# Kernel optimization log

Hardware: AMD Instinct MI355X
Metric: run time of the kernel (lower is better)

The kernel has to match this reference:

```python
import jax, jax.numpy as jnp
import numpy as np

EPS = 1e-5  # BatchNorm2d default eps

def setup_inputs() -> dict:
    key = jax.random.key(0)
    k1, k2, k3, k4 = jax.random.split(key, 4)
    B, Cin, Cout, T, V = 64, 64, 128, 300, 25
    x = jax.random.normal(k1, (B, Cin, T, V), dtype=jnp.float32)
    adj = jax.random.uniform(k2, (V, V), dtype=jnp.float32)
    # Conv2d(kernel_size=1) weight (Cout, Cin), kaiming-ish scale
    W = jax.random.normal(k3, (Cout, Cin), dtype=jnp.float32) * (1.0 / np.sqrt(Cin))
    b = jnp.zeros((Cout,), dtype=jnp.float32)
    gamma = jnp.ones((Cout,), dtype=jnp.float32)
    beta = jnp.zeros((Cout,), dtype=jnp.float32)
    return {"x": x, "adj": adj, "W": W, "b": b, "gamma": gamma, "beta": beta}

def reference(x, adj, W, b, gamma, beta):
    # x: (B, C, T, V); graph aggregation over joints: matmul with adj on last dim
    xg = jnp.einsum('bctv,vw->bctw', x, adj)
    # 1x1 conv == per-(t,v) channel projection
    y = jnp.einsum('bctv,oc->botv', xg, W) + b[None, :, None, None]
    # BatchNorm2d (training mode): per-channel stats over (B, T, V), biased var
    mean = jnp.mean(y, axis=(0, 2, 3), keepdims=True)
    var = jnp.mean((y - mean) ** 2, axis=(0, 2, 3), keepdims=True)
    yn = (y - mean) * jax.lax.rsqrt(var + EPS)
    out = jax.nn.relu(gamma[None, :, None, None] * yn + beta[None, :, None, None])
    return out
```

## Files before the change

### kernel.cpp

```cpp
#include <hip/hip_runtime.h>
#include <stdint.h>

typedef __attribute__((ext_vector_type(8)))  short   short8;
typedef __attribute__((ext_vector_type(4)))  short   short4v;
typedef __attribute__((ext_vector_type(16))) float   floatx16;

#define B_    64
#define CIN   64
#define COUT  128
#define T_    300
#define V_    25
#define TV    (T_ * V_)
#define NRED  (B_ * T_ * V_)
#define NSLOTS 32
#define EPS   1e-5f


__device__ __forceinline__ unsigned short f2bf(float f) {
    union { float f; uint32_t u; } c; c.f = f;
    uint32_t u = c.u;
    u += 0x7FFFu + ((u >> 16) & 1u);
    return (unsigned short)(u >> 16);
}

__device__ __forceinline__ floatx16 fzero16() {
    floatx16 z;
#pragma unroll
    for (int i = 0; i < 16; ++i) z[i] = 0.f;
    return z;
}

__global__ void pack_kernel(const float* __restrict__ W, const float* __restrict__ adj,
                            unsigned short* __restrict__ wsW, unsigned short* __restrict__ wsAdj) {
    int stride = blockDim.x * gridDim.x;
    for (int idx = threadIdx.x + blockIdx.x * blockDim.x; idx < 8192; idx += stride) {
        int j  = idx & 7;
        int l  = (idx >> 3) & 63;
        int kk = (idx >> 9) & 3;
        int w  = idx >> 11;
        int o  = 32 * w + (l & 31);
        int c  = 16 * kk + 8 * (l >> 5) + j;
        wsW[idx] = f2bf(W[o * CIN + c]);
    }
    for (int idx = threadIdx.x + blockIdx.x * blockDim.x; idx < 1024; idx += stride) {
        int j = idx & 7;
        int l = (idx >> 3) & 63;
        int s = idx >> 9;
        int k = 16 * s + 8 * (l >> 5) + j;
        int n = l & 31;
        float v = (k < V_ && n < V_) ? adj[k * V_ + n] : 0.f;
        wsAdj[idx] = f2bf(v);
    }
}

template <bool WRITE>
__global__ __launch_bounds__(256) void main_kernel(
    const float* __restrict__ x,
    const unsigned short* __restrict__ wsW,
    const unsigned short* __restrict__ wsAdj,
    const float* __restrict__ scale, const float* __restrict__ shift,
    float* __restrict__ psum, float* __restrict__ psq,
    float* __restrict__ out)
{
    __shared__ unsigned short Gbuf[2][2048] __attribute__((aligned(16)));

    const int tid  = threadIdx.x;
    const int wave = tid >> 6;
    const int lane = tid & 63;
    const int q    = lane >> 5;
    const int ln   = lane & 31;
    const int b    = blockIdx.y;
    const int t0   = blockIdx.x * 4;
    const int ctile = wave & 1;
    const int tsel  = wave >> 1;

    short8 wf[4];
#pragma unroll
    for (int kk = 0; kk < 4; ++kk)
        wf[kk] = ((const short8*)wsW)[(wave * 4 + kk) * 64 + lane];
    short8 af[2];
#pragma unroll
    for (int s = 0; s < 2; ++s)
        af[s] = ((const short8*)wsAdj)[s * 64 + lane];

    float sc[16], sh[16], sums[16], sqs[16];
    if (WRITE) {
#pragma unroll
        for (int r = 0; r < 16; ++r) {
            int row = 32 * wave + (r & 3) + 8 * (r >> 2) + 4 * q;
            sc[r] = scale[row];
            sh[r] = shift[row];
        }
    } else {
#pragma unroll
        for (int r = 0; r < 16; ++r) { sums[r] = 0.f; sqs[r] = 0.f; }
    }

    for (int iter = 0; iter < 2; ++iter) {
        const int t = t0 + iter * 2 + tsel;
        const float* xrow = x + ((size_t)(b * CIN + 32 * ctile + ln) * T_ + t) * V_;

        short8 xa0, xa1;
#pragma unroll
        for (int j = 0; j < 8; ++j) xa0[j] = (short)f2bf(xrow[8 * q + j]);
        if (q == 0) {
#pragma unroll
            for (int j = 0; j < 8; ++j) xa1[j] = (short)f2bf(xrow[16 + j]);
        } else {
            xa1[0] = (short)f2bf(xrow[24]);
#pragma unroll
            for (int j = 1; j < 8; ++j) xa1[j] = 0;
        }

        floatx16 g = fzero16();
        g = __builtin_amdgcn_mfma_f32_32x32x16_bf16(xa0, af[0], g, 0, 0, 0);
        g = __builtin_amdgcn_mfma_f32_32x32x16_bf16(xa1, af[1], g, 0, 0, 0);

        __syncthreads();

#pragma unroll
        for (int r1 = 0; r1 < 4; ++r1) {
            short4v p;
#pragma unroll
            for (int r0 = 0; r0 < 4; ++r0) p[r0] = (short)f2bf(g[r1 * 4 + r0]);
            *(short4v*)&Gbuf[tsel][((4 * ctile + r1) * 32 + ln) * 8 + 4 * q] = p;
        }

        __syncthreads();

#pragma unroll
        for (int ts = 0; ts < 2; ++ts) {
            floatx16 acc = fzero16();
#pragma unroll
            for (int kk = 0; kk < 4; ++kk) {
                short8 bfrag = *(const short8*)&Gbuf[ts][((kk * 2 + q) * 32 + ln) * 8];
                acc = __builtin_amdgcn_mfma_f32_32x32x16_bf16(wf[kk], bfrag, acc, 0, 0, 0);
            }
            if (WRITE) {
                const int t_out = t0 + iter * 2 + ts;
                if (ln < V_) {
                    float* obase = out + ((size_t)(b * COUT + 32 * wave) * T_ + t_out) * V_ + ln;
#pragma unroll
                    for (int r = 0; r < 16; ++r) {
                        int row = (r & 3) + 8 * (r >> 2) + 4 * q;
                        float v = sc[r] * acc[r] + sh[r];
                        obase[(size_t)row * TV] = v > 0.f ? v : 0.f;
                    }
                }
            } else {
#pragma unroll
                for (int r = 0; r < 16; ++r) {
                    sums[r] += acc[r];
                    sqs[r]  += acc[r] * acc[r];
                }
            }
        }
    }

    if (!WRITE) {
#pragma unroll
        for (int r = 0; r < 16; ++r) {
            float s = sums[r], ss = sqs[r];
#pragma unroll
            for (int m = 1; m <= 16; m <<= 1) {
                s  += __shfl_xor(s,  m, 64);
                ss += __shfl_xor(ss, m, 64);
            }
            sums[r] = s; sqs[r] = ss;
        }
        if (ln == 0) {
            int slot = (blockIdx.y * 75 + blockIdx.x) & (NSLOTS - 1);
#pragma unroll
            for (int r = 0; r < 16; ++r) {
                int ch = 32 * wave + (r & 3) + 8 * (r >> 2) + 4 * q;
                atomicAdd(&psum[slot * COUT + ch], sums[r]);
                atomicAdd(&psq [slot * COUT + ch], sqs[r]);
            }
        }
    }
}

__global__ void stats_kernel(const float* __restrict__ psum, const float* __restrict__ psq,
                             const float* __restrict__ gamma, const float* __restrict__ beta,
                             float* __restrict__ scale, float* __restrict__ shift) {
    int o = threadIdx.x;
    float s = 0.f, ss = 0.f;
    for (int k = 0; k < NSLOTS; ++k) {
        s  += psum[k * COUT + o];
        ss += psq [k * COUT + o];
    }
    float mean = s / (float)NRED;
    float var  = ss / (float)NRED - mean * mean;
    float inv  = rsqrtf(var + EPS);
    float scv  = gamma[o] * inv;
    scale[o] = scv;
    shift[o] = beta[o] - mean * scv;
}

extern "C" void kernel_launch(void* const* d_in, const int* in_sizes, int n_in,
                              void* d_out, int out_size, void* d_ws, size_t ws_size,
                              hipStream_t stream) {
    const float* x     = (const float*)d_in[0];
    const float* adj   = (const float*)d_in[1];
    const float* W     = (const float*)d_in[2];
    const float* gamma = (const float*)d_in[4];
    const float* beta  = (const float*)d_in[5];
    float* out = (float*)d_out;

    char* ws = (char*)d_ws;
    unsigned short* wsW   = (unsigned short*)(ws);
    unsigned short* wsAdj = (unsigned short*)(ws + 16384);
    float* psum  = (float*)(ws + 18432);
    float* psq   = (float*)(ws + 34816);
    float* scale = (float*)(ws + 51200);
    float* shift = (float*)(ws + 51712);

    hipMemsetAsync(psum, 0, 2 * NSLOTS * COUT * sizeof(float), stream);

    pack_kernel<<<8, 256, 0, stream>>>(W, adj, wsW, wsAdj);

    dim3 grid(75, 64);
    main_kernel<false><<<grid, 256, 0, stream>>>(x, wsW, wsAdj, nullptr, nullptr, psum, psq, nullptr);
    stats_kernel<<<1, 128, 0, stream>>>(psum, psq, gamma, beta, scale, shift);
    main_kernel<true><<<grid, 256, 0, stream>>>(x, wsW, wsAdj, scale, shift, psum, psq, out);
}
```

Before: 464.6 us.

## Reorder to channel projection before graph aggregation, fuse packing and stats kernels

Computes W·x first and then multiplies by adj (associativity), keeping the intermediate in registers and rearranging it across lanes with a shuffle, which removes the LDS buffer and its barriers. Weight and adjacency fragments are built inside each kernel, so the pack kernel goes away, and the stats reduction is folded into the second pass, removing the stats kernel. Each block now covers 12 timesteps instead of 4, and output stores are vectorized along the joint dimension. The trade-offs are extra shuffles and redundant stats and fragment work per block, plus strided scalar loads of x.

```diff
diff --git a/kernel.cpp b/kernel.cpp
--- a/kernel.cpp
+++ b/kernel.cpp
@@ -1,26 +1,26 @@
 #include <hip/hip_runtime.h>
+#include <hip/hip_bf16.h>
 #include <stdint.h>
 
 typedef __attribute__((ext_vector_type(8)))  short   short8;
-typedef __attribute__((ext_vector_type(4)))  short   short4v;
 typedef __attribute__((ext_vector_type(16))) float   floatx16;
+typedef __attribute__((ext_vector_type(4)))  float   floatx4;
 
 #define B_    64
 #define CIN   64
 #define COUT  128
 #define T_    300
 #define V_    25
-#define TV    (T_ * V_)
 #define NRED  (B_ * T_ * V_)
 #define NSLOTS 32
+#define NT    12
 #define EPS   1e-5f
 
 
-__device__ __forceinline__ unsigned short f2bf(float f) {
-    union { float f; uint32_t u; } c; c.f = f;
-    uint32_t u = c.u;
-    u += 0x7FFFu + ((u >> 16) & 1u);
-    return (unsigned short)(u >> 16);
+__device__ __forceinline__ uint32_t pk2(float a, float b) {
+    union { __hip_bfloat162 h; uint32_t u; } c;
+    c.h = __float22bfloat162_rn(make_float2(a, b));
+    return c.u;
 }
 
 __device__ __forceinline__ floatx16 fzero16() {
@@ -30,171 +30,179 @@
     return z;
 }
 
-__global__ void pack_kernel(const float* __restrict__ W, const float* __restrict__ adj,
-                            unsigned short* __restrict__ wsW, unsigned short* __restrict__ wsAdj) {
-    int stride = blockDim.x * gridDim.x;
-    for (int idx = threadIdx.x + blockIdx.x * blockDim.x; idx < 8192; idx += stride) {
-        int j  = idx & 7;
-        int l  = (idx >> 3) & 63;
-        int kk = (idx >> 9) & 3;
-        int w  = idx >> 11;
-        int o  = 32 * w + (l & 31);
-        int c  = 16 * kk + 8 * (l >> 5) + j;
-        wsW[idx] = f2bf(W[o * CIN + c]);
-    }
-    for (int idx = threadIdx.x + blockIdx.x * blockDim.x; idx < 1024; idx += stride) {
-        int j = idx & 7;
-        int l = (idx >> 3) & 63;
-        int s = idx >> 9;
-        int k = 16 * s + 8 * (l >> 5) + j;
-        int n = l & 31;
-        float v = (k < V_ && n < V_) ? adj[k * V_ + n] : 0.f;
-        wsAdj[idx] = f2bf(v);
-    }
-}
-
-template <bool WRITE>
-__global__ __launch_bounds__(256) void main_kernel(
-    const float* __restrict__ x,
-    const unsigned short* __restrict__ wsW,
-    const unsigned short* __restrict__ wsAdj,
-    const float* __restrict__ scale, const float* __restrict__ shift,
-    float* __restrict__ psum, float* __restrict__ psq,
-    float* __restrict__ out)
+__device__ __forceinline__ void cvt_hb(const floatx16 h, int q, short8 hb[2]) {
+    uint32_t pk[8], pp[8];
+#pragma unroll
+    for (int i = 0; i < 8; ++i) pk[i] = pk2(h[2 * i], h[2 * i + 1]);
+#pragma unroll
+    for (int i = 0; i < 8; ++i) pp[i] = (uint32_t)__shfl_xor((int)pk[i], 32, 64);
+#pragma unroll
+    for (int s = 0; s < 2; ++s) {
+        union { short8 sv; uint32_t u[4]; } F;
+        F.u[0] = q ? pp[4 * s + 2] : pk[4 * s];
+        F.u[1] = q ? pp[4 * s + 3] : pk[4 * s + 1];
+        F.u[2] = q ? pk[4 * s + 2] : pp[4 * s];
+        F.u[3] = q ? pk[4 * s + 3] : pp[4 * s + 1];
+        hb[s] = F.sv;
+    }
+}
+
+__device__ __forceinline__ void build_const_frags(const float* __restrict__ W,
+                                                  const float* __restrict__ adj,
+                                                  int wave, int ln, int q,
+                                                  short8 wf[4], short8 af[2]) {
+    const float* wr = W + (32 * wave + ln) * CIN;
+#pragma unroll
+    for (int kk = 0; kk < 4; ++kk) {
+        int c0 = 16 * kk + 8 * q;
+        floatx4 a = *(const floatx4*)(wr + c0);
+        floatx4 b = *(const floatx4*)(wr + c0 + 4);
+        union { short8 sv; uint32_t u[4]; } F;
+        F.u[0] = pk2(a[0], a[1]); F.u[1] = pk2(a[2], a[3]);
+        F.u[2] = pk2(b[0], b[1]); F.u[3] = pk2(b[2], b[3]);
+        wf[kk] = F.sv;
+    }
+#pragma unroll
+    for (int s = 0; s < 2; ++s) {
+        union { short8 sv; uint32_t u[4]; } F;
+#pragma unroll
+        for (int p = 0; p < 4; ++p) {
+            int v0 = 16 * s + 8 * q + 2 * p;
+            float e0 = (v0     < V_ && ln < V_) ? adj[v0 * V_ + ln]       : 0.f;
+            float e1 = (v0 + 1 < V_ && ln < V_) ? adj[(v0 + 1) * V_ + ln] : 0.f;
+            F.u[p] = pk2(e0, e1);
+        }
+        af[s] = F.sv;
+    }
+}
+
+__device__ __forceinline__ void build_xa(const float* __restrict__ x,
+                                         int base_u, int loff, short8 xa[4]) {
+#pragma unroll
+    for (int kk = 0; kk < 4; ++kk) {
+        union { short8 sv; uint32_t u[4]; } F;
+#pragma unroll
+        for (int p = 0; p < 4; ++p) {
+            float e0 = x[base_u + (16 * kk + 2 * p) * (T_ * V_) + loff];
+            float e1 = x[base_u + (16 * kk + 2 * p + 1) * (T_ * V_) + loff];
+            F.u[p] = pk2(e0, e1);
+        }
+        xa[kk] = F.sv;
+    }
+}
+
+__device__ __forceinline__ floatx16 compute_yt(const short8 xa[4], const short8 wf[4],
+                                               const short8 af[2], int q) {
+    floatx16 h = fzero16();
+#pragma unroll
+    for (int kk = 0; kk < 4; ++kk)
+        h = __builtin_amdgcn_mfma_f32_32x32x16_bf16(xa[kk], wf[kk], h, 0, 0, 0);
+    short8 hb[2];
+    cvt_hb(h, q, hb);
+    floatx16 y = fzero16();
+#pragma unroll
+    for (int s = 0; s < 2; ++s)
+        y = __builtin_amdgcn_mfma_f32_32x32x16_bf16(af[s], hb[s], y, 0, 0, 0);
+    return y;
+}
+
+__global__ __launch_bounds__(256, 3) void pass1_kernel(
+    const float* __restrict__ x, const float* __restrict__ adj,
+    const float* __restrict__ W,
+    float* __restrict__ psum, float* __restrict__ psq)
 {
-    __shared__ unsigned short Gbuf[2][2048] __attribute__((aligned(16)));
-
     const int tid  = threadIdx.x;
     const int wave = tid >> 6;
     const int lane = tid & 63;
     const int q    = lane >> 5;
     const int ln   = lane & 31;
     const int b    = blockIdx.y;
-    const int t0   = blockIdx.x * 4;
-    const int ctile = wave & 1;
-    const int tsel  = wave >> 1;
-
-    short8 wf[4];
-#pragma unroll
-    for (int kk = 0; kk < 4; ++kk)
-        wf[kk] = ((const short8*)wsW)[(wave * 4 + kk) * 64 + lane];
-    short8 af[2];
-#pragma unroll
-    for (int s = 0; s < 2; ++s)
-        af[s] = ((const short8*)wsAdj)[s * 64 + lane];
-
-    float sc[16], sh[16], sums[16], sqs[16];
-    if (WRITE) {
-#pragma unroll
-        for (int r = 0; r < 16; ++r) {
-            int row = 32 * wave + (r & 3) + 8 * (r >> 2) + 4 * q;
-            sc[r] = scale[row];
-            sh[r] = shift[row];
-        }
-    } else {
-#pragma unroll
-        for (int r = 0; r < 16; ++r) { sums[r] = 0.f; sqs[r] = 0.f; }
-    }
-
-    for (int iter = 0; iter < 2; ++iter) {
-        const int t = t0 + iter * 2 + tsel;
-        const float* xrow = x + ((size_t)(b * CIN + 32 * ctile + ln) * T_ + t) * V_;
-
-        short8 xa0, xa1;
-#pragma unroll
-        for (int j = 0; j < 8; ++j) xa0[j] = (short)f2bf(xrow[8 * q + j]);
+    const int tbase = blockIdx.x * NT;
+
+    short8 wf[4], af[2];
+    build_const_frags(W, adj, wave, ln, q, wf, af);
+
+    const int vcl  = ln < V_ ? ln : V_ - 1;
+    const int loff = vcl + q * 8 * (T_ * V_);
+
+    float sum = 0.f, sq = 0.f;
+    for (int i = 0; i < NT; ++i) {
+        const int t = tbase + i;
+        const int base_u = b * (CIN * T_ * V_) + t * V_;
+        short8 xa[4];
+        build_xa(x, base_u, loff, xa);
+        floatx16 y = compute_yt(xa, wf, af, q);
+#pragma unroll
+        for (int r = 0; r < 16; ++r) { sum += y[r]; sq += y[r] * y[r]; }
+    }
+
+    sum += __shfl_xor(sum, 32, 64);
+    sq  += __shfl_xor(sq,  32, 64);
+    if (q == 0) {
+        int slot = (blockIdx.y * 25 + blockIdx.x) & (NSLOTS - 1);
+        atomicAdd(&psum[slot * COUT + 32 * wave + ln], sum);
+        atomicAdd(&psq [slot * COUT + 32 * wave + ln], sq);
+    }
+}
+
+__global__ __launch_bounds__(256, 3) void pass2_kernel(
+    const float* __restrict__ x, const float* __restrict__ adj,
+    const float* __restrict__ W,
+    const float* __restrict__ gamma, const float* __restrict__ beta,
+    const float* __restrict__ psum, const float* __restrict__ psq,
+    float* __restrict__ out)
+{
+    const int tid  = threadIdx.x;
+    const int wave = tid >> 6;
+    const int lane = tid & 63;
+    const int q    = lane >> 5;
+    const int ln   = lane & 31;
+    const int b    = blockIdx.y;
+    const int tbase = blockIdx.x * NT;
+    const int o_l  = 32 * wave + ln;
+
+    short8 wf[4], af[2];
+    build_const_frags(W, adj, wave, ln, q, wf, af);
+
+    float s = 0.f, ss = 0.f;
+#pragma unroll 4
+    for (int k = 0; k < NSLOTS; ++k) {
+        s  += psum[k * COUT + o_l];
+        ss += psq [k * COUT + o_l];
+    }
+    const float mean = s / (float)NRED;
+    const float var  = ss / (float)NRED - mean * mean;
+    const float inv  = rsqrtf(var + EPS);
+    const float sc   = gamma[o_l] * inv;
+    const float sh   = beta[o_l] - mean * sc;
+
+    const int vcl  = ln < V_ ? ln : V_ - 1;
+    const int loff = vcl + q * 8 * (T_ * V_);
+    const int po   = o_l * (T_ * V_) + 4 * q;
+
+    for (int i = 0; i < NT; ++i) {
+        const int t = tbase + i;
+        const int base_u = b * (CIN * T_ * V_) + t * V_;
+        short8 xa[4];
+        build_xa(x, base_u, loff, xa);
+        floatx16 y = compute_yt(xa, wf, af, q);
+
+        float* ob = out + (size_t)(b * (COUT * T_ * V_) + t * V_);
+#pragma unroll
+        for (int g = 0; g < 3; ++g) {
+            float tmp[4];
+#pragma unroll
+            for (int j = 0; j < 4; ++j) {
+                float v = sc * y[4 * g + j] + sh;
+                tmp[j] = v > 0.f ? v : 0.f;
+            }
+            __builtin_memcpy(&ob[po + 8 * g], tmp, 16);
+        }
         if (q == 0) {
-#pragma unroll
-            for (int j = 0; j < 8; ++j) xa1[j] = (short)f2bf(xrow[16 + j]);
-        } else {
-            xa1[0] = (short)f2bf(xrow[24]);
-#pragma unroll
-            for (int j = 1; j < 8; ++j) xa1[j] = 0;
-        }
-
-        floatx16 g = fzero16();
-        g = __builtin_amdgcn_mfma_f32_32x32x16_bf16(xa0, af[0], g, 0, 0, 0);
-        g = __builtin_amdgcn_mfma_f32_32x32x16_bf16(xa1, af[1], g, 0, 0, 0);
-
-        __syncthreads();
-
-#pragma unroll
-        for (int r1 = 0; r1 < 4; ++r1) {
-            short4v p;
-#pragma unroll
-            for (int r0 = 0; r0 < 4; ++r0) p[r0] = (short)f2bf(g[r1 * 4 + r0]);
-            *(short4v*)&Gbuf[tsel][((4 * ctile + r1) * 32 + ln) * 8 + 4 * q] = p;
-        }
-
-        __syncthreads();
-
-#pragma unroll
-        for (int ts = 0; ts < 2; ++ts) {
-            floatx16 acc = fzero16();
-#pragma unroll
-            for (int kk = 0; kk < 4; ++kk) {
-                short8 bfrag = *(const short8*)&Gbuf[ts][((kk * 2 + q) * 32 + ln) * 8];
-                acc = __builtin_amdgcn_mfma_f32_32x32x16_bf16(wf[kk], bfrag, acc, 0, 0, 0);
-            }
-            if (WRITE) {
-                const int t_out = t0 + iter * 2 + ts;
-                if (ln < V_) {
-                    float* obase = out + ((size_t)(b * COUT + 32 * wave) * T_ + t_out) * V_ + ln;
-#pragma unroll
-                    for (int r = 0; r < 16; ++r) {
-                        int row = (r & 3) + 8 * (r >> 2) + 4 * q;
-                        float v = sc[r] * acc[r] + sh[r];
-                        obase[(size_t)row * TV] = v > 0.f ? v : 0.f;
-                    }
-                }
-            } else {
-#pragma unroll
-                for (int r = 0; r < 16; ++r) {
-                    sums[r] += acc[r];
-                    sqs[r]  += acc[r] * acc[r];
-                }
-            }
-        }
-    }
-
-    if (!WRITE) {
-#pragma unroll
-        for (int r = 0; r < 16; ++r) {
-            float s = sums[r], ss = sqs[r];
-#pragma unroll
-            for (int m = 1; m <= 16; m <<= 1) {
-                s  += __shfl_xor(s,  m, 64);
-                ss += __shfl_xor(ss, m, 64);
-            }
-            sums[r] = s; sqs[r] = ss;
-        }
-        if (ln == 0) {
-            int slot = (blockIdx.y * 75 + blockIdx.x) & (NSLOTS - 1);
-#pragma unroll
-            for (int r = 0; r < 16; ++r) {
-                int ch = 32 * wave + (r & 3) + 8 * (r >> 2) + 4 * q;
-                atomicAdd(&psum[slot * COUT + ch], sums[r]);
-                atomicAdd(&psq [slot * COUT + ch], sqs[r]);
-            }
-        }
-    }
-}
-
-__global__ void stats_kernel(const float* __restrict__ psum, const float* __restrict__ psq,
-                             const float* __restrict__ gamma, const float* __restrict__ beta,
-                             float* __restrict__ scale, float* __restrict__ shift) {
-    int o = threadIdx.x;
-    float s = 0.f, ss = 0.f;
-    for (int k = 0; k < NSLOTS; ++k) {
-        s  += psum[k * COUT + o];
-        ss += psq [k * COUT + o];
-    }
-    float mean = s / (float)NRED;
-    float var  = ss / (float)NRED - mean * mean;
-    float inv  = rsqrtf(var + EPS);
-    float scv  = gamma[o] * inv;
-    scale[o] = scv;
-    shift[o] = beta[o] - mean * scv;
+            float v = sc * y[12] + sh;
+            ob[po + 24] = v > 0.f ? v : 0.f;
+        }
+    }
 }
 
 extern "C" void kernel_launch(void* const* d_in, const int* in_sizes, int n_in,
@@ -207,20 +215,12 @@
     const float* beta  = (const float*)d_in[5];
     float* out = (float*)d_out;
 
-    char* ws = (char*)d_ws;
-    unsigned short* wsW   = (unsigned short*)(ws);
-    unsigned short* wsAdj = (unsigned short*)(ws + 16384);
-    float* psum  = (float*)(ws + 18432);
-    float* psq   = (float*)(ws + 34816);
-    float* scale = (float*)(ws + 51200);
-    float* shift = (float*)(ws + 51712);
+    float* psum = (float*)d_ws;
+    float* psq  = (float*)((char*)d_ws + NSLOTS * COUT * sizeof(float));
 
     hipMemsetAsync(psum, 0, 2 * NSLOTS * COUT * sizeof(float), stream);
 
-    pack_kernel<<<8, 256, 0, stream>>>(W, adj, wsW, wsAdj);
-
-    dim3 grid(75, 64);
-    main_kernel<false><<<grid, 256, 0, stream>>>(x, wsW, wsAdj, nullptr, nullptr, psum, psq, nullptr);
-    stats_kernel<<<1, 128, 0, stream>>>(psum, psq, gamma, beta, scale, shift);
-    main_kernel<true><<<grid, 256, 0, stream>>>(x, wsW, wsAdj, scale, shift, psum, psq, out);
-}
+    dim3 grid(T_ / NT, B_);
+    pass1_kernel<<<grid, 256, 0, stream>>>(x, adj, W, psum, psq);
+    pass2_kernel<<<grid, 256, 0, stream>>>(x, adj, W, gamma, beta, psum, psq, out);
+}
```

Measured after the change: 564.2 us. 21.4% more time.
